# Kernel optimization log

Hardware: AMD Instinct MI355X
Metric: run time of the kernel (lower is better)

The kernel has to match this reference:

```python
import jax, jax.numpy as jnp
import numpy as np

N_PFAS, N_GW, N_SW = 20000, 100000, 30000
D, OUT = 128, 128
E_PG, E_GP, E_PS, E_SP = 1600000, 640000, 480000, 320000


def setup_inputs() -> dict:
    key = jax.random.key(0)
    ks = jax.random.split(key, 32)
    g = lambda k, shape, fan_in: jax.random.normal(k, shape, jnp.float32) / np.sqrt(fan_in)
    inp = {
        "x_pfas": jax.random.normal(ks[0], (N_PFAS, D), jnp.float32),
        "x_gw": jax.random.normal(ks[1], (N_GW, D), jnp.float32),
        "x_sw": jax.random.normal(ks[2], (N_SW, D), jnp.float32),
        "ei_pg_src": jax.random.randint(ks[3], (E_PG,), 0, N_PFAS),
        "ei_pg_dst": jax.random.randint(ks[4], (E_PG,), 0, N_GW),
        "ei_gp_src": jax.random.randint(ks[5], (E_GP,), 0, N_GW),
        "ei_gp_dst": jax.random.randint(ks[6], (E_GP,), 0, N_PFAS),
        "ei_ps_src": jax.random.randint(ks[7], (E_PS,), 0, N_PFAS),
        "ei_ps_dst": jax.random.randint(ks[8], (E_PS,), 0, N_SW),
        "ei_sp_src": jax.random.randint(ks[9], (E_SP,), 0, N_SW),
        "ei_sp_dst": jax.random.randint(ks[10], (E_SP,), 0, N_PFAS),
    }
    # SAGEConv params per relation: lin_l (on aggregated neighbors, with bias), lin_r (root, no bias)
    names = ["pg", "gp", "ps", "sp"]
    for i, n in enumerate(names):
        inp[f"Wl_{n}"] = g(ks[11 + 3 * i], (D, OUT), D)
        inp[f"bl_{n}"] = jnp.zeros((OUT,), jnp.float32)
        inp[f"Wr_{n}"] = g(ks[12 + 3 * i], (D, OUT), D)
    inp["W_gw"] = g(ks[25], (OUT, 1), OUT)
    inp["b_gw"] = jnp.zeros((1,), jnp.float32)
    inp["W_sw"] = g(ks[26], (OUT, 1), OUT)
    inp["b_sw"] = jnp.zeros((1,), jnp.float32)
    return inp


def _sage(x_src, x_dst, src, dst, n_dst, Wl, bl, Wr):
    # SAGEConv: lin_l(mean_j x_src[j]) + lin_r(x_dst)
    msg = x_src[src]  # [E, D] gather
    s = jax.ops.segment_sum(msg, dst, num_segments=n_dst)
    cnt = jax.ops.segment_sum(jnp.ones((src.shape[0],), x_src.dtype), dst, num_segments=n_dst)
    mean = s / jnp.maximum(cnt, 1.0)[:, None]
    return mean @ Wl + bl + x_dst @ Wr


def reference(x_pfas, x_gw, x_sw,
              ei_pg_src, ei_pg_dst, ei_gp_src, ei_gp_dst,
              ei_ps_src, ei_ps_dst, ei_sp_src, ei_sp_dst,
              Wl_pg, bl_pg, Wr_pg, Wl_gp, bl_gp, Wr_gp,
              Wl_ps, bl_ps, Wr_ps, Wl_sp, bl_sp, Wr_sp,
              W_gw, b_gw, W_sw, b_sw):
    h_gw = _sage(x_pfas, x_gw, ei_pg_src, ei_pg_dst, N_GW, Wl_pg, bl_pg, Wr_pg)
    h_sw = _sage(x_pfas, x_sw, ei_ps_src, ei_ps_dst, N_SW, Wl_ps, bl_ps, Wr_ps)
    # pfas_sites is the destination of two relations -> HeteroConv aggr='sum'
    h_pf = (_sage(x_gw, x_pfas, ei_gp_src, ei_gp_dst, N_PFAS, Wl_gp, bl_gp, Wr_gp)
            + _sage(x_sw, x_pfas, ei_sp_src, ei_sp_dst, N_PFAS, Wl_sp, bl_sp, Wr_sp))
    h_pf = jax.nn.relu(h_pf)
    h_gw = jax.nn.relu(h_gw)
    h_sw = jax.nn.relu(h_sw)
    out_gw = h_gw @ W_gw + b_gw   # [N_GW, 1]
    out_sw = h_sw @ W_sw + b_sw   # [N_SW, 1]
    return h_pf, out_gw, out_sw
```

## Files before the change

kernel.cpp:

```cpp
#include <hip/hip_runtime.h>

#define N_PFAS 20000
#define N_GW   100000
#define N_SW   30000
#define E_PG   1600000
#define E_GP   640000
#define E_PS   480000
#define E_SP   320000
#define E_TOT  (E_PG + E_PS + E_GP + E_SP)
#define BASE_PG 0
#define BASE_PS (N_GW)
#define BASE_GP (N_GW + N_SW)
#define BASE_SP (N_GW + N_SW + N_PFAS)
#define NTOT    (N_GW + N_SW + 2 * N_PFAS)
#define NB        ((NTOT + 255) / 256)
#define SEG_CAP   9216
#define BIN_EPT   12
#define BIN_EPB   (256 * BIN_EPT)
#define BIN_NBLK  ((E_TOT + BIN_EPB - 1) / BIN_EPB)
#define T64_PF ((N_PFAS + 63) / 64)
#define T64_GW ((N_GW + 63) / 64)
#define T64_SW ((N_SW + 63) / 64)
#define T64_ALL (T64_PF + T64_GW + T64_SW)
#define SEGP_BLKS (N_PFAS / 16)
#define GW_BLKS   ((N_GW + 31) / 32)
#define SW_BLKS   ((N_SW + 31) / 32)
#define SSTR 136

typedef _Float16 h2_t  __attribute__((ext_vector_type(2)));
typedef _Float16 f16x4 __attribute__((ext_vector_type(4)));
typedef _Float16 f16x8 __attribute__((ext_vector_type(8)));
typedef float    f32x4 __attribute__((ext_vector_type(4)));
union HU { unsigned u; h2_t h; };
__device__ __forceinline__ h2_t u2h2(unsigned u) { HU x; x.u = u; return x.h; }

__device__ __forceinline__ void gather_sum_f16(
    const unsigned short* __restrict__ bufT16, const int* __restrict__ perm,
    int lo, int hi, int tx, h2_t& tl, h2_t& th)
{
    h2_t hz; hz.x = (_Float16)0.f; hz.y = (_Float16)0.f;
    h2_t a0 = hz, a1 = hz, a2 = hz, a3 = hz, a4 = hz, a5 = hz, a6 = hz, a7 = hz;
    int i = lo;
    for (; i + 8 <= hi; i += 8) {
        uint2 v0 = *(const uint2*)(bufT16 + (size_t)perm[i + 0] * 128 + tx * 4);
        uint2 v1 = *(const uint2*)(bufT16 + (size_t)perm[i + 1] * 128 + tx * 4);
        uint2 v2 = *(const uint2*)(bufT16 + (size_t)perm[i + 2] * 128 + tx * 4);
        uint2 v3 = *(const uint2*)(bufT16 + (size_t)perm[i + 3] * 128 + tx * 4);
        uint2 v4 = *(const uint2*)(bufT16 + (size_t)perm[i + 4] * 128 + tx * 4);
        uint2 v5 = *(const uint2*)(bufT16 + (size_t)perm[i + 5] * 128 + tx * 4);
        uint2 v6 = *(const uint2*)(bufT16 + (size_t)perm[i + 6] * 128 + tx * 4);
        uint2 v7 = *(const uint2*)(bufT16 + (size_t)perm[i + 7] * 128 + tx * 4);
        a0 += u2h2(v0.x); a1 += u2h2(v0.y);
        a2 += u2h2(v1.x); a3 += u2h2(v1.y);
        a4 += u2h2(v2.x); a5 += u2h2(v2.y);
        a6 += u2h2(v3.x); a7 += u2h2(v3.y);
        a0 += u2h2(v4.x); a1 += u2h2(v4.y);
        a2 += u2h2(v5.x); a3 += u2h2(v5.y);
        a4 += u2h2(v6.x); a5 += u2h2(v6.y);
        a6 += u2h2(v7.x); a7 += u2h2(v7.y);
    }
    for (; i + 2 <= hi; i += 2) {
        uint2 v0 = *(const uint2*)(bufT16 + (size_t)perm[i + 0] * 128 + tx * 4);
        uint2 v1 = *(const uint2*)(bufT16 + (size_t)perm[i + 1] * 128 + tx * 4);
        a0 += u2h2(v0.x); a1 += u2h2(v0.y);
        a2 += u2h2(v1.x); a3 += u2h2(v1.y);
    }
    if (i < hi) {
        uint2 v0 = *(const uint2*)(bufT16 + (size_t)perm[i] * 128 + tx * 4);
        a0 += u2h2(v0.x); a1 += u2h2(v0.y);
    }
    tl = (a0 + a2) + (a4 + a6);
    th = (a1 + a3) + (a5 + a7);
}

__global__ __launch_bounds__(256) void prep_wt_kernel(
    const float* __restrict__ Wl_pg, const float* __restrict__ Wl_ps,
    const float* __restrict__ Wr_gp, const float* __restrict__ Wr_sp,
    const float* __restrict__ Wl_gp, const float* __restrict__ Wr_pg,
    const float* __restrict__ Wl_sp, const float* __restrict__ Wr_ps,
    _Float16* __restrict__ WtF_pg, _Float16* __restrict__ WtF_ps,
    _Float16* __restrict__ WtFR_pf,
    _Float16* __restrict__ WtF_gp, _Float16* __restrict__ WtFR_gw,
    _Float16* __restrict__ WtF_sp, _Float16* __restrict__ WtFR_sw,
    int* __restrict__ gcursor, int* __restrict__ off_all)
{
    const int m = blockIdx.x >> 2;
    const int chunk = blockIdx.x & 3;
    if (blockIdx.x == 0) {
        for (int i = threadIdx.x; i < NB; i += 256) gcursor[i] = 0;
        if (threadIdx.x == 0) off_all[NTOT] = E_TOT;
    }
    const float* A = nullptr; const float* B = nullptr; _Float16* O = nullptr;
    switch (m) {
        case 0: A = Wl_pg; O = WtF_pg;  break;
        case 1: A = Wl_ps; O = WtF_ps;  break;
        case 2: A = Wr_gp; B = Wr_sp; O = WtFR_pf; break;
        case 3: A = Wl_gp; O = WtF_gp;  break;
        case 4: A = Wr_pg; O = WtFR_gw; break;
        case 5: A = Wl_sp; O = WtF_sp;  break;
        default: A = Wr_ps; O = WtFR_sw; break;
    }
    for (int t = chunk * 512 + threadIdx.x; t < (chunk + 1) * 512; t += 256) {
        int lane = t & 63, g = t >> 6;
        int ks = g & 3, ct = g >> 2;
        int nn = ct * 16 + (lane & 15);
        int k0 = ks * 32 + (lane >> 4) * 8;
        f16x8 v;
#pragma unroll
        for (int j = 0; j < 8; ++j) {
            float x = A[(k0 + j) * 128 + nn];
            if (B) x += B[(k0 + j) * 128 + nn];
            v[j] = (_Float16)x;
        }
        *(f16x8*)(O + (size_t)t * 8) = v;
    }
}

__device__ __forceinline__ void mfma_one_B16(
    const _Float16* __restrict__ WtF, const f16x8* a, _Float16* sstage,
    int rbase, int n, int lane, _Float16* __restrict__ o16)
{
    f32x4 acc[8];
#pragma unroll
    for (int ct = 0; ct < 8; ++ct) acc[ct] = (f32x4){0.f, 0.f, 0.f, 0.f};
#pragma unroll
    for (int ct = 0; ct < 8; ++ct) {
        f16x8 b0 = *(const f16x8*)(WtF + (size_t)((ct * 4 + 0) * 64 + lane) * 8);
        f16x8 b1 = *(const f16x8*)(WtF + (size_t)((ct * 4 + 1) * 64 + lane) * 8);
        f16x8 b2 = *(const f16x8*)(WtF + (size_t)((ct * 4 + 2) * 64 + lane) * 8);
        f16x8 b3 = *(const f16x8*)(WtF + (size_t)((ct * 4 + 3) * 64 + lane) * 8);
        acc[ct] = __builtin_amdgcn_mfma_f32_16x16x32_f16(a[0], b0, acc[ct], 0, 0, 0);
        acc[ct] = __builtin_amdgcn_mfma_f32_16x16x32_f16(a[1], b1, acc[ct], 0, 0, 0);
        acc[ct] = __builtin_amdgcn_mfma_f32_16x16x32_f16(a[2], b2, acc[ct], 0, 0, 0);
        acc[ct] = __builtin_amdgcn_mfma_f32_16x16x32_f16(a[3], b3, acc[ct], 0, 0, 0);
    }

    const int rl = (lane >> 4) * 4;
    const int cb = lane & 15;
#pragma unroll
    for (int ct = 0; ct < 8; ++ct)
#pragma unroll
        for (int e = 0; e < 4; ++e)
            sstage[(rl + e) * SSTR + ct * 16 + cb] = (_Float16)acc[ct][e];

#pragma unroll
    for (int i = 0; i < 4; ++i) {
        int lr = i * 4 + (lane >> 4);
        int r = rbase + lr;
        if (r < n) {
            f16x8 v = *(const f16x8*)(sstage + lr * SSTR + cb * 8);
            *(f16x8*)(o16 + ((size_t)r << 7) + cb * 8) = v;
        }
    }
}

__device__ __forceinline__ void mfma_one_B32(
    const _Float16* __restrict__ WtF, const f16x8* a,
    int rbase, int n, int lane, float* __restrict__ o32)
{
    f32x4 acc[8];
#pragma unroll
    for (int ct = 0; ct < 8; ++ct) acc[ct] = (f32x4){0.f, 0.f, 0.f, 0.f};
#pragma unroll
    for (int ct = 0; ct < 8; ++ct) {
        f16x8 b0 = *(const f16x8*)(WtF + (size_t)((ct * 4 + 0) * 64 + lane) * 8);
        f16x8 b1 = *(const f16x8*)(WtF + (size_t)((ct * 4 + 1) * 64 + lane) * 8);
        f16x8 b2 = *(const f16x8*)(WtF + (size_t)((ct * 4 + 2) * 64 + lane) * 8);
        f16x8 b3 = *(const f16x8*)(WtF + (size_t)((ct * 4 + 3) * 64 + lane) * 8);
        acc[ct] = __builtin_amdgcn_mfma_f32_16x16x32_f16(a[0], b0, acc[ct], 0, 0, 0);
        acc[ct] = __builtin_amdgcn_mfma_f32_16x16x32_f16(a[1], b1, acc[ct], 0, 0, 0);
        acc[ct] = __builtin_amdgcn_mfma_f32_16x16x32_f16(a[2], b2, acc[ct], 0, 0, 0);
        acc[ct] = __builtin_amdgcn_mfma_f32_16x16x32_f16(a[3], b3, acc[ct], 0, 0, 0);
    }
    const int rowb = rbase + (lane >> 4) * 4;
    const int bcol = lane & 15;
#pragma unroll
    for (int ct = 0; ct < 8; ++ct) {
        const int col = ct * 16 + bcol;
#pragma unroll
        for (int e = 0; e < 4; ++e) {
            int r = rowb + e;
            if (r < n) o32[((size_t)r << 7) + col] = acc[ct][e];
        }
    }
}

__global__ __launch_bounds__(256, 4) void trans_bin_kernel(
    const float* __restrict__ x_pfas, const float* __restrict__ x_gw,
    const float* __restrict__ x_sw,
    const _Float16* __restrict__ WtF_pg, const _Float16* __restrict__ WtF_ps,
    const _Float16* __restrict__ WtFR_pf,
    const _Float16* __restrict__ WtF_gp, const _Float16* __restrict__ WtFR_gw,
    const _Float16* __restrict__ WtF_sp, const _Float16* __restrict__ WtFR_sw,
    _Float16* __restrict__ bufT_pg, _Float16* __restrict__ bufT_ps,
    float* __restrict__ R_pf,
    _Float16* __restrict__ bufT_gp, _Float16* __restrict__ R_gw,
    _Float16* __restrict__ bufT_sp, _Float16* __restrict__ R_sw,
    const int* __restrict__ s_pg, const int* __restrict__ d_pg,
    const int* __restrict__ s_ps, const int* __restrict__ d_ps,
    const int* __restrict__ s_gp, const int* __restrict__ d_gp,
    const int* __restrict__ s_sp, const int* __restrict__ d_sp,
    int* __restrict__ gcursor, unsigned* __restrict__ pairs)
{
    __shared__ char smem[4 * 16 * SSTR * 2];
    const int tid = threadIdx.x;

    if (blockIdx.x < BIN_NBLK) {
        int* hist = (int*)smem;
        int* chunkBase = hist + NB;
        for (int i = tid; i < NB; i += 256) hist[i] = 0;
        __syncthreads();

        const int base = blockIdx.x * BIN_EPB;
        int bkt[BIN_EPT], rnk[BIN_EPT];
        unsigned pk[BIN_EPT];
#pragma unroll
        for (int k = 0; k < BIN_EPT; ++k) {
            int e = base + k * 256 + tid;
            int idx = -1, src = 0;
            if (e < E_PG) { idx = BASE_PG + d_pg[e]; src = s_pg[e]; }
            else if (e < E_PG + E_PS) { int i2 = e - E_PG; idx = BASE_PS + d_ps[i2]; src = s_ps[i2]; }
            else if (e < E_PG + E_PS + E_GP) { int i2 = e - E_PG - E_PS; idx = BASE_GP + d_gp[i2]; src = s_gp[i2]; }
            else if (e < E_TOT) { int i2 = e - E_PG - E_PS - E_GP; idx = BASE_SP + d_sp[i2]; src = s_sp[i2]; }
            if (idx >= 0) {
                int b = idx >> 8;
                bkt[k] = b;
                rnk[k] = atomicAdd(&hist[b], 1);
                pk[k] = (unsigned)(idx & 255) | ((unsigned)src << 8);
            } else bkt[k] = -1;
        }
        __syncthreads();
        for (int i = tid; i < NB; i += 256) {
            int c = hist[i];
            chunkBase[i] = c ? atomicAdd(&gcursor[i], c) : 0;
        }
        __syncthreads();
#pragma unroll
        for (int k = 0; k < BIN_EPT; ++k) {
            if (bkt[k] >= 0) {
                int slot = chunkBase[bkt[k]] + rnk[k];
                if (slot < SEG_CAP)
                    pairs[(size_t)bkt[k] * SEG_CAP + slot] = pk[k];
            }
        }
        return;
    }

    const int b = blockIdx.x - BIN_NBLK;
    int mode, tile, n; const float* X;
    if (b < T64_PF)               { mode = 0; tile = b;                    X = x_pfas; n = N_PFAS; }
    else if (b < T64_PF + T64_GW) { mode = 1; tile = b - T64_PF;           X = x_gw;   n = N_GW; }
    else                          { mode = 2; tile = b - T64_PF - T64_GW;  X = x_sw;   n = N_SW; }
    const int lane = tid & 63;
    const int w    = tid >> 6;
    const int rbase = tile * 64 + w * 16;
    _Float16* sX = (_Float16*)smem + (size_t)w * 16 * SSTR;

    const float* Xt = X + (size_t)rbase * 128;
    const int rows_left = n - rbase;
#pragma unroll
    for (int t = 0; t < 8; ++t) {
        int idx = t * 64 + lane;
        int rr = idx >> 5, c4 = idx & 31;
        float4 xv = make_float4(0.f, 0.f, 0.f, 0.f);
        if (rr < rows_left) xv = *(const float4*)(Xt + rr * 128 + c4 * 4);
        f16x4 v;
        v[0] = (_Float16)xv.x; v[1] = (_Float16)xv.y;
        v[2] = (_Float16)xv.z; v[3] = (_Float16)xv.w;
        *(f16x4*)(sX + rr * SSTR + c4 * 4) = v;
    }
    f16x8 a[4];
#pragma unroll
    for (int ks = 0; ks < 4; ++ks)
        a[ks] = *(const f16x8*)(sX + (lane & 15) * SSTR + ks * 32 + (lane >> 4) * 8);

    if (mode == 0) {
        mfma_one_B16(WtF_pg,  a, sX, rbase, n, lane, bufT_pg);
        mfma_one_B16(WtF_ps,  a, sX, rbase, n, lane, bufT_ps);
        mfma_one_B32(WtFR_pf, a, rbase, n, lane, R_pf);
    } else if (mode == 1) {
        mfma_one_B16(WtF_gp,  a, sX, rbase, n, lane, bufT_gp);
        mfma_one_B16(WtFR_gw, a, sX, rbase, n, lane, R_gw);
    } else {
        mfma_one_B16(WtF_sp,  a, sX, rbase, n, lane, bufT_sp);
        mfma_one_B16(WtFR_sw, a, sX, rbase, n, lane, R_sw);
    }
}

__global__ __launch_bounds__(512) void unbin_kernel(
    const unsigned* __restrict__ pairs, const int* __restrict__ gcursor,
    int* __restrict__ off_all, int* __restrict__ perm_all)
{
    __shared__ int sPerm[SEG_CAP];
    __shared__ int cnt[256];
    __shared__ int sp[256];
    __shared__ int cur[256];
    const int b = blockIdx.x;
    const int nb0 = b << 8;
    const int nb1 = min(nb0 + 256, NTOT);
    const int tid = threadIdx.x;

    int* red = sPerm;
    int part = 0;
    for (int i = tid; i < b; i += 512) part += gcursor[i];
    red[tid] = part;
    __syncthreads();
    for (int ofs = 256; ofs > 0; ofs >>= 1) {
        if (tid < ofs) red[tid] += red[tid + ofs];
        __syncthreads();
    }
    const int obase = red[0];
    int len = gcursor[b];
    if (len > SEG_CAP) len = SEG_CAP;
    const unsigned* reg = pairs + (size_t)b * SEG_CAP;

    if (tid < 256) cnt[tid] = 0;
    __syncthreads();
    for (int i = tid; i < len; i += 512)
        atomicAdd(&cnt[reg[i] & 255u], 1);
    __syncthreads();
    int v = (tid < 256) ? cnt[tid] : 0;
    if (tid < 256) sp[tid] = v;
    __syncthreads();
    for (int ofs = 1; ofs < 256; ofs <<= 1) {
        int add = (tid < 256 && tid >= ofs) ? sp[tid - ofs] : 0;
        __syncthreads();
        if (tid < 256) sp[tid] += add;
        __syncthreads();
    }
    if (tid < 256) {
        int excl = sp[tid] - v;
        cur[tid] = excl;
        if (nb0 + tid < nb1) off_all[nb0 + tid] = obase + excl;
    }
    __syncthreads();

    for (int i = tid; i < len; i += 512) {
        unsigned p = reg[i];
        int pos = atomicAdd(&cur[p & 255u], 1);
        sPerm[pos] = (int)(p >> 8);
    }
    __syncthreads();
    for (int i = tid; i < len; i += 512)
        perm_all[obase + i] = sPerm[i];
}

__global__ __launch_bounds__(512, 8) void gather_all_kernel(
    const _Float16* __restrict__ R_gw, const _Float16* __restrict__ R_sw,
    const float* __restrict__ bl_pg, const float* __restrict__ bl_ps,
    const unsigned short* __restrict__ bufT_pg,
    const unsigned short* __restrict__ bufT_ps,
    const unsigned short* __restrict__ bufT_gp,
    const unsigned short* __restrict__ bufT_sp,
    const int* __restrict__ perm, const int* __restrict__ off_all,
    const float* __restrict__ W_gw, const float* __restrict__ b_gw,
    const float* __restrict__ W_sw, const float* __restrict__ b_sw,
    float* __restrict__ o_gw, float* __restrict__ o_sw,
    const float* __restrict__ R_pf,
    const float* __restrict__ bl_gp, const float* __restrict__ bl_sp,
    float* __restrict__ h_pf)
{
    const int b = blockIdx.x;
    const int tid = threadIdx.x;
    const int tx = tid & 31;
    const int g = tid >> 5;

    if (b < SEGP_BLKS) {
        const int node = b * 16 + g;
        int loG = off_all[BASE_GP + node], hiG = off_all[BASE_GP + node + 1];
        h2_t tlG, thG;
        gather_sum_f16(bufT_gp, perm, loG, hiG, tx, tlG, thG);
        int loS = off_all[BASE_SP + node], hiS = off_all[BASE_SP + node + 1];
        h2_t tlS, thS;
        gather_sum_f16(bufT_sp, perm, loS, hiS, tx, tlS, thS);
        float invG = 1.0f / fmaxf((float)(hiG - loG), 1.0f);
        float invS = 1.0f / fmaxf((float)(hiS - loS), 1.0f);
        float4 rv = ((const float4*)R_pf)[(size_t)node * 32 + tx];
        float4 b1 = ((const float4*)bl_gp)[tx];
        float4 b2 = ((const float4*)bl_sp)[tx];
        float4 o;
        o.x = fmaxf(rv.x + (float)tlG.x * invG + (float)tlS.x * invS + b1.x + b2.x, 0.f);
        o.y = fmaxf(rv.y + (float)tlG.y * invG + (float)tlS.y * invS + b1.y + b2.y, 0.f);
        o.z = fmaxf(rv.z + (float)thG.x * invG + (float)thS.x * invS + b1.z + b2.z, 0.f);
        o.w = fmaxf(rv.w + (float)thG.y * invG + (float)thS.y * invS + b1.w + b2.w, 0.f);
        ((float4*)h_pf)[(size_t)node * 32 + tx] = o;
    } else {
        const int bb = b - SEGP_BLKS;
        int n; const _Float16* R; const float* bl; const unsigned short* bufT16;
        const int* off; const float* wout; const float* bout; float* out; int tile;
        if (bb < GW_BLKS) {
            n = N_GW; R = R_gw; bl = bl_pg; bufT16 = bufT_pg; off = off_all + BASE_PG;
            wout = W_gw; bout = b_gw; out = o_gw; tile = bb;
        } else {
            n = N_SW; R = R_sw; bl = bl_ps; bufT16 = bufT_ps; off = off_all + BASE_PS;
            wout = W_sw; bout = b_sw; out = o_sw; tile = bb - GW_BLKS;
        }
        const int rbase = tile * 32 + g * 2;
        float4 bv = ((const float4*)bl)[tx];
        float4 wo = ((const float4*)wout)[tx];
        float bo = bout[0];
#pragma unroll
        for (int rr = 0; rr < 2; ++rr) {
            int r = rbase + rr;
            int lo = 0, hi = 0;
            if (r < n) { lo = off[r]; hi = off[r + 1]; }
            h2_t tl, th;
            gather_sum_f16(bufT16, perm, lo, hi, tx, tl, th);
            float4 rf = make_float4(0.f, 0.f, 0.f, 0.f);
            if (r < n) {
                uint2 rv = *(const uint2*)((const unsigned short*)R + ((size_t)r << 7) + tx * 4);
                h2_t r01 = u2h2(rv.x), r23 = u2h2(rv.y);
                rf = make_float4((float)r01.x, (float)r01.y, (float)r23.x, (float)r23.y);
            }
            float inv = 1.0f / fmaxf((float)(hi - lo), 1.0f);
            float h0  = fmaxf(rf.x + bv.x + (float)tl.x * inv, 0.f);
            float h1  = fmaxf(rf.y + bv.y + (float)tl.y * inv, 0.f);
            float h2v = fmaxf(rf.z + bv.z + (float)th.x * inv, 0.f);
            float h3  = fmaxf(rf.w + bv.w + (float)th.y * inv, 0.f);
            float pv = h0 * wo.x + h1 * wo.y + h2v * wo.z + h3 * wo.w;
            pv += __shfl_xor(pv, 1, 32);
            pv += __shfl_xor(pv, 2, 32);
            pv += __shfl_xor(pv, 4, 32);
            pv += __shfl_xor(pv, 8, 32);
            pv += __shfl_xor(pv, 16, 32);
            if (tx == 0 && r < n) out[r] = pv + bo;
        }
    }
}

extern "C" void kernel_launch(void* const* d_in, const int* in_sizes, int n_in,
                              void* d_out, int out_size, void* d_ws, size_t ws_size,
                              hipStream_t stream)
{
    const float* x_pfas = (const float*)d_in[0];
    const float* x_gw   = (const float*)d_in[1];
    const float* x_sw   = (const float*)d_in[2];
    const int* ei_pg_src = (const int*)d_in[3];
    const int* ei_pg_dst = (const int*)d_in[4];
    const int* ei_gp_src = (const int*)d_in[5];
    const int* ei_gp_dst = (const int*)d_in[6];
    const int* ei_ps_src = (const int*)d_in[7];
    const int* ei_ps_dst = (const int*)d_in[8];
    const int* ei_sp_src = (const int*)d_in[9];
    const int* ei_sp_dst = (const int*)d_in[10];
    const float* Wl_pg = (const float*)d_in[11];
    const float* bl_pg = (const float*)d_in[12];
    const float* Wr_pg = (const float*)d_in[13];
    const float* Wl_gp = (const float*)d_in[14];
    const float* bl_gp = (const float*)d_in[15];
    const float* Wr_gp = (const float*)d_in[16];
    const float* Wl_ps = (const float*)d_in[17];
    const float* bl_ps = (const float*)d_in[18];
    const float* Wr_ps = (const float*)d_in[19];
    const float* Wl_sp = (const float*)d_in[20];
    const float* bl_sp = (const float*)d_in[21];
    const float* Wr_sp = (const float*)d_in[22];
    const float* W_gw = (const float*)d_in[23];
    const float* b_gw = (const float*)d_in[24];
    const float* W_sw = (const float*)d_in[25];
    const float* b_sw = (const float*)d_in[26];

    float* out  = (float*)d_out;
    float* h_pf = out;
    float* o_gw = out + (size_t)N_PFAS * 128;
    float* o_sw = o_gw + N_GW;

    char* p = (char*)d_ws;
    auto alloc = [&](size_t bytes) { char* q = p; p += (bytes + 15) & ~(size_t)15; return q; };
    unsigned short* bufT_pg = (unsigned short*)alloc((size_t)N_PFAS * 128 * 2);
    unsigned short* bufT_ps = (unsigned short*)alloc((size_t)N_PFAS * 128 * 2);
    unsigned short* bufT_gp = (unsigned short*)alloc((size_t)N_GW * 128 * 2);
    unsigned short* bufT_sp = (unsigned short*)alloc((size_t)N_SW * 128 * 2);
    _Float16* R_gw = (_Float16*)alloc((size_t)N_GW * 128 * 2);
    _Float16* R_sw = (_Float16*)alloc((size_t)N_SW * 128 * 2);
    float* R_pf = (float*)alloc((size_t)N_PFAS * 128 * 4);
    int* perm_all   = (int*)alloc((size_t)E_TOT * 4);
    unsigned* pairs = (unsigned*)alloc((size_t)NB * SEG_CAP * 4);
    int* off_all    = (int*)alloc((size_t)(NTOT + 1) * 4);
    int* gcursor    = (int*)alloc((size_t)NB * 4);
    _Float16* WtF_pg  = (_Float16*)alloc(16384 * 2);
    _Float16* WtF_ps  = (_Float16*)alloc(16384 * 2);
    _Float16* WtFR_pf = (_Float16*)alloc(16384 * 2);
    _Float16* WtF_gp  = (_Float16*)alloc(16384 * 2);
    _Float16* WtFR_gw = (_Float16*)alloc(16384 * 2);
    _Float16* WtF_sp  = (_Float16*)alloc(16384 * 2);
    _Float16* WtFR_sw = (_Float16*)alloc(16384 * 2);

    prep_wt_kernel<<<28, 256, 0, stream>>>(
        Wl_pg, Wl_ps, Wr_gp, Wr_sp, Wl_gp, Wr_pg, Wl_sp, Wr_ps,
        WtF_pg, WtF_ps, WtFR_pf, WtF_gp, WtFR_gw, WtF_sp, WtFR_sw,
        gcursor, off_all);

    trans_bin_kernel<<<BIN_NBLK + T64_ALL, 256, 0, stream>>>(
        x_pfas, x_gw, x_sw,
        WtF_pg, WtF_ps, WtFR_pf, WtF_gp, WtFR_gw, WtF_sp, WtFR_sw,
        (_Float16*)bufT_pg, (_Float16*)bufT_ps, R_pf,
        (_Float16*)bufT_gp, R_gw, (_Float16*)bufT_sp, R_sw,
        ei_pg_src, ei_pg_dst, ei_ps_src, ei_ps_dst,
        ei_gp_src, ei_gp_dst, ei_sp_src, ei_sp_dst,
        gcursor, pairs);

    unbin_kernel<<<NB, 512, 0, stream>>>(pairs, gcursor, off_all, perm_all);

    gather_all_kernel<<<SEGP_BLKS + GW_BLKS + SW_BLKS, 512, 0, stream>>>(
        R_gw, R_sw, bl_pg, bl_ps, bufT_pg, bufT_ps, bufT_gp, bufT_sp,
        perm_all, off_all, W_gw, b_gw, W_sw, b_sw, o_gw, o_sw,
        R_pf, bl_gp, bl_sp, h_pf);
}
```

Before: 349.2 us.

## Split transform blocks per weight matrix and stage weights in LDS

```diff
diff --git a/kernel.cpp b/kernel.cpp
--- a/kernel.cpp
+++ b/kernel.cpp
@@ -21,7 +21,7 @@
 #define T64_PF ((N_PFAS + 63) / 64)
 #define T64_GW ((N_GW + 63) / 64)
 #define T64_SW ((N_SW + 63) / 64)
-#define T64_ALL (T64_PF + T64_GW + T64_SW)
+#define PROD_BLKS (3 * T64_PF + 2 * T64_GW + 2 * T64_SW)
 #define SEGP_BLKS (N_PFAS / 16)
 #define GW_BLKS   ((N_GW + 31) / 32)
 #define SW_BLKS   ((N_SW + 31) / 32)
@@ -116,8 +116,8 @@
     }
 }
 
-__device__ __forceinline__ void mfma_one_B16(
-    const _Float16* __restrict__ WtF, const f16x8* a, _Float16* sstage,
+__device__ __forceinline__ void mfma_lds_B16(
+    const _Float16* sW, const f16x8* a, _Float16* sstage,
     int rbase, int n, int lane, _Float16* __restrict__ o16)
 {
     f32x4 acc[8];
@@ -125,10 +125,10 @@
     for (int ct = 0; ct < 8; ++ct) acc[ct] = (f32x4){0.f, 0.f, 0.f, 0.f};
 #pragma unroll
     for (int ct = 0; ct < 8; ++ct) {
-        f16x8 b0 = *(const f16x8*)(WtF + (size_t)((ct * 4 + 0) * 64 + lane) * 8);
-        f16x8 b1 = *(const f16x8*)(WtF + (size_t)((ct * 4 + 1) * 64 + lane) * 8);
-        f16x8 b2 = *(const f16x8*)(WtF + (size_t)((ct * 4 + 2) * 64 + lane) * 8);
-        f16x8 b3 = *(const f16x8*)(WtF + (size_t)((ct * 4 + 3) * 64 + lane) * 8);
+        f16x8 b0 = *(const f16x8*)(sW + ((ct * 4 + 0) * 64 + lane) * 8);
+        f16x8 b1 = *(const f16x8*)(sW + ((ct * 4 + 1) * 64 + lane) * 8);
+        f16x8 b2 = *(const f16x8*)(sW + ((ct * 4 + 2) * 64 + lane) * 8);
+        f16x8 b3 = *(const f16x8*)(sW + ((ct * 4 + 3) * 64 + lane) * 8);
         acc[ct] = __builtin_amdgcn_mfma_f32_16x16x32_f16(a[0], b0, acc[ct], 0, 0, 0);
         acc[ct] = __builtin_amdgcn_mfma_f32_16x16x32_f16(a[1], b1, acc[ct], 0, 0, 0);
         acc[ct] = __builtin_amdgcn_mfma_f32_16x16x32_f16(a[2], b2, acc[ct], 0, 0, 0);
@@ -154,8 +154,8 @@
     }
 }
 
-__device__ __forceinline__ void mfma_one_B32(
-    const _Float16* __restrict__ WtF, const f16x8* a,
+__device__ __forceinline__ void mfma_lds_B32(
+    const _Float16* sW, const f16x8* a,
     int rbase, int n, int lane, float* __restrict__ o32)
 {
     f32x4 acc[8];
@@ -163,10 +163,10 @@
     for (int ct = 0; ct < 8; ++ct) acc[ct] = (f32x4){0.f, 0.f, 0.f, 0.f};
 #pragma unroll
     for (int ct = 0; ct < 8; ++ct) {
-        f16x8 b0 = *(const f16x8*)(WtF + (size_t)((ct * 4 + 0) * 64 + lane) * 8);
-        f16x8 b1 = *(const f16x8*)(WtF + (size_t)((ct * 4 + 1) * 64 + lane) * 8);
-        f16x8 b2 = *(const f16x8*)(WtF + (size_t)((ct * 4 + 2) * 64 + lane) * 8);
-        f16x8 b3 = *(const f16x8*)(WtF + (size_t)((ct * 4 + 3) * 64 + lane) * 8);
+        f16x8 b0 = *(const f16x8*)(sW + ((ct * 4 + 0) * 64 + lane) * 8);
+        f16x8 b1 = *(const f16x8*)(sW + ((ct * 4 + 1) * 64 + lane) * 8);
+        f16x8 b2 = *(const f16x8*)(sW + ((ct * 4 + 2) * 64 + lane) * 8);
+        f16x8 b3 = *(const f16x8*)(sW + ((ct * 4 + 3) * 64 + lane) * 8);
         acc[ct] = __builtin_amdgcn_mfma_f32_16x16x32_f16(a[0], b0, acc[ct], 0, 0, 0);
         acc[ct] = __builtin_amdgcn_mfma_f32_16x16x32_f16(a[1], b1, acc[ct], 0, 0, 0);
         acc[ct] = __builtin_amdgcn_mfma_f32_16x16x32_f16(a[2], b2, acc[ct], 0, 0, 0);
@@ -185,7 +185,7 @@
     }
 }
 
-__global__ __launch_bounds__(256, 4) void trans_bin_kernel(
+__global__ __launch_bounds__(256, 2) void trans_bin_kernel(
     const float* __restrict__ x_pfas, const float* __restrict__ x_gw,
     const float* __restrict__ x_sw,
     const _Float16* __restrict__ WtF_pg, const _Float16* __restrict__ WtF_ps,
@@ -202,7 +202,7 @@
     const int* __restrict__ s_sp, const int* __restrict__ d_sp,
     int* __restrict__ gcursor, unsigned* __restrict__ pairs)
 {
-    __shared__ char smem[4 * 16 * SSTR * 2];
+    __shared__ char smem[32768 + 4 * 16 * SSTR * 2];
     const int tid = threadIdx.x;
 
     if (blockIdx.x < BIN_NBLK) {
@@ -246,15 +246,33 @@
         return;
     }
 
-    const int b = blockIdx.x - BIN_NBLK;
-    int mode, tile, n; const float* X;
-    if (b < T64_PF)               { mode = 0; tile = b;                    X = x_pfas; n = N_PFAS; }
-    else if (b < T64_PF + T64_GW) { mode = 1; tile = b - T64_PF;           X = x_gw;   n = N_GW; }
-    else                          { mode = 2; tile = b - T64_PF - T64_GW;  X = x_sw;   n = N_SW; }
+    const int b2 = blockIdx.x - BIN_NBLK;
+    int tile, sub, n; const float* X;
+    const _Float16* WtF; _Float16* o16 = nullptr; float* o32 = nullptr;
+    if (b2 < 3 * T64_PF) {
+        tile = b2 / 3; sub = b2 - tile * 3; X = x_pfas; n = N_PFAS;
+        if (sub == 0)      { WtF = WtF_pg;  o16 = bufT_pg; }
+        else if (sub == 1) { WtF = WtF_ps;  o16 = bufT_ps; }
+        else               { WtF = WtFR_pf; o32 = R_pf; }
+    } else if (b2 < 3 * T64_PF + 2 * T64_GW) {
+        int t = b2 - 3 * T64_PF;
+        tile = t >> 1; sub = t & 1; X = x_gw; n = N_GW;
+        if (sub == 0) { WtF = WtF_gp;  o16 = bufT_gp; }
+        else          { WtF = WtFR_gw; o16 = R_gw; }
+    } else {
+        int t = b2 - 3 * T64_PF - 2 * T64_GW;
+        tile = t >> 1; sub = t & 1; X = x_sw; n = N_SW;
+        if (sub == 0) { WtF = WtF_sp;  o16 = bufT_sp; }
+        else          { WtF = WtFR_sw; o16 = R_sw; }
+    }
     const int lane = tid & 63;
     const int w    = tid >> 6;
     const int rbase = tile * 64 + w * 16;
-    _Float16* sX = (_Float16*)smem + (size_t)w * 16 * SSTR;
+    _Float16* sW = (_Float16*)smem;
+    _Float16* sX = (_Float16*)(smem + 32768) + (size_t)w * 16 * SSTR;
+
+    for (int t = tid; t < 2048; t += 256)
+        *(f16x8*)(sW + t * 8) = *(const f16x8*)(WtF + (size_t)t * 8);
 
     const float* Xt = X + (size_t)rbase * 128;
     const int rows_left = n - rbase;
@@ -273,18 +291,10 @@
 #pragma unroll
     for (int ks = 0; ks < 4; ++ks)
         a[ks] = *(const f16x8*)(sX + (lane & 15) * SSTR + ks * 32 + (lane >> 4) * 8);
-
-    if (mode == 0) {
-        mfma_one_B16(WtF_pg,  a, sX, rbase, n, lane, bufT_pg);
-        mfma_one_B16(WtF_ps,  a, sX, rbase, n, lane, bufT_ps);
-        mfma_one_B32(WtFR_pf, a, rbase, n, lane, R_pf);
-    } else if (mode == 1) {
-        mfma_one_B16(WtF_gp,  a, sX, rbase, n, lane, bufT_gp);
-        mfma_one_B16(WtFR_gw, a, sX, rbase, n, lane, R_gw);
-    } else {
-        mfma_one_B16(WtF_sp,  a, sX, rbase, n, lane, bufT_sp);
-        mfma_one_B16(WtFR_sw, a, sX, rbase, n, lane, R_sw);
-    }
+    __syncthreads();
+
+    if (o32) mfma_lds_B32(sW, a, rbase, n, lane, o32);
+    else     mfma_lds_B16(sW, a, sX, rbase, n, lane, o16);
 }
 
 __global__ __launch_bounds__(512) void unbin_kernel(
@@ -491,7 +501,7 @@
         WtF_pg, WtF_ps, WtFR_pf, WtF_gp, WtFR_gw, WtF_sp, WtFR_sw,
         gcursor, off_all);
 
-    trans_bin_kernel<<<BIN_NBLK + T64_ALL, 256, 0, stream>>>(
+    trans_bin_kernel<<<BIN_NBLK + PROD_BLKS, 256, 0, stream>>>(
         x_pfas, x_gw, x_sw,
         WtF_pg, WtF_ps, WtFR_pf, WtF_gp, WtFR_gw, WtF_sp, WtFR_sw,
         (_Float16*)bufT_pg, (_Float16*)bufT_ps, R_pf,
```

Measured after the change: 373.6 us. +7.0%, slower.
